# Performance work log

Measured on AMD Instinct MI355X. Metric: run time of the kernel, lower is better.

The kernel has to match this reference:

```python
import jax, jax.numpy as jnp
import numpy as np

EPS = 1e-5

def _ln(x, g, b):
    m = jnp.mean(x, axis=-1, keepdims=True)
    v = jnp.var(x, axis=-1, keepdims=True)
    return (x - m) / jnp.sqrt(v + EPS) * g + b

def setup_inputs() -> dict:
    key = jax.random.key(0)
    ks = jax.random.split(key, 16)
    B, N, CZ, C = 1, 512, 128, 16
    s_cz = 1.0 / np.sqrt(CZ)
    s_c = 1.0 / np.sqrt(C)
    def lin(k, fan_in, shape):
        return jax.random.uniform(k, shape, jnp.float32, -1.0, 1.0) / np.sqrt(fan_in)
    return {
        'x': jax.random.normal(ks[0], (B, N, N, CZ), jnp.float32),
        'Wa1': lin(ks[1], CZ, (CZ, C)), 'ba1': lin(ks[2], CZ, (C,)),
        'Wa2': lin(ks[3], CZ, (CZ, C)), 'ba2': lin(ks[4], CZ, (C,)),
        'Wb1': lin(ks[5], CZ, (CZ, C)), 'bb1': lin(ks[6], CZ, (C,)),
        'Wb2': lin(ks[7], CZ, (CZ, C)), 'bb2': lin(ks[8], CZ, (C,)),
        'ln2_g': jnp.ones((C,), jnp.float32), 'ln2_b': jnp.zeros((C,), jnp.float32),
        'Wg': lin(ks[9], CZ, (CZ, CZ)), 'bg': lin(ks[10], CZ, (CZ,)),
        'Wz': lin(ks[11], C, (C, CZ)), 'bz': lin(ks[12], C, (CZ,)),
    }

def reference(x, Wa1, ba1, Wa2, ba2, Wb1, bb1, Wb2, bb2, ln2_g, ln2_b, Wg, bg, Wz, bz):
    # NOTE: original code computes z=ln1(x) then overwrites z=x, so ln1 is a no-op.
    direction = 'outgoing'
    a = jax.nn.sigmoid((x @ Wa1 + ba1) * (x @ Wa2 + ba2))  # [B,N,N,c]
    b = jax.nn.sigmoid((x @ Wb1 + bb1) * (x @ Wb2 + bb2))  # [B,N,N,c]
    if direction == 'incoming':
        a = jnp.swapaxes(a, 1, 2)
        b = jnp.swapaxes(b, 1, 2)
    g = jax.nn.sigmoid(x @ Wg + bg)  # [B,N,N,c_z]
    # z[b,i,j,c] = sum_k a[b,i,k,c] * b[b,k,j,c]  (per-channel triangle matmul)
    z = jnp.einsum('bikc,bkjc->bijc', a, b)
    return g * (_ln(z, ln2_g, ln2_b) @ Wz + bz)
```

## Files before the change

### kernel.cpp

```cpp
#include <hip/hip_runtime.h>


#define NN 512
#define PP (NN*NN)
#define CZD 128
#define CD 16
#define LN_EPS 1e-5f

typedef unsigned short u16;
typedef __bf16 bf16x8 __attribute__((ext_vector_type(8)));
typedef float  f32x4  __attribute__((ext_vector_type(4)));

#define OFF_A  0u
#define OFF_B  8388608u
#define OFF_Z  16777216u
#define OFF_G  33554432u
#define OFF_WT 100663296u
#define OFF_BC 100712448u

__device__ __forceinline__ float bf2f(u16 u) {
    union { unsigned int i; float f; } v; v.i = ((unsigned int)u) << 16; return v.f;
}
__device__ __forceinline__ u16 f2bf(float f) {
    union { float f; unsigned int i; } v; v.f = f;
    unsigned int r = (v.i + 0x7FFFu + ((v.i >> 16) & 1u)) >> 16;
    return (u16)r;
}
__device__ __forceinline__ float sigmoidf(float x) { return 1.0f / (1.0f + __expf(-x)); }

__global__ void pack_w(const float* __restrict__ Wa1, const float* __restrict__ Wa2,
                       const float* __restrict__ Wb1, const float* __restrict__ Wb2,
                       const float* __restrict__ Wg,
                       const float* __restrict__ ba1, const float* __restrict__ ba2,
                       const float* __restrict__ bb1, const float* __restrict__ bb2,
                       const float* __restrict__ bg,
                       u16* __restrict__ wt, float* __restrict__ bc) {
    int idx = blockIdx.x * 256 + threadIdx.x;
    int n = idx >> 7, k = idx & 127;
    float v;
    if      (n < 16) v = Wa1[k * CD + n];
    else if (n < 32) v = Wa2[k * CD + (n - 16)];
    else if (n < 48) v = Wb1[k * CD + (n - 32)];
    else if (n < 64) v = Wb2[k * CD + (n - 48)];
    else             v = Wg [k * CZD + (n - 64)];
    wt[n * CZD + k] = f2bf(v);
    if (idx < 192) {
        float b;
        if      (idx < 16) b = ba1[idx];
        else if (idx < 32) b = ba2[idx - 16];
        else if (idx < 48) b = bb1[idx - 32];
        else if (idx < 64) b = bb2[idx - 48];
        else               b = bg [idx - 64];
        bc[idx] = b;
    }
}

__global__ __launch_bounds__(256) void proj_kernel(const float* __restrict__ x,
                                                   const u16* __restrict__ wt,
                                                   const float* __restrict__ bc,
                                                   u16* __restrict__ a_ws, u16* __restrict__ b_ws,
                                                   u16* __restrict__ g_ws) {
    __shared__ __align__(16) u16 Xlds[32][136];
    const int t = threadIdx.x;
    const int wave = t >> 6, lane = t & 63;
    const int l16 = lane & 15, quad = lane >> 4;
    const int rt = wave & 1, cg = wave >> 1;
    const long rowBase = (long)blockIdx.x * 32;

#pragma unroll
    for (int i = 0; i < 2; ++i) {
        int chunk = t + 256 * i;
        int r = chunk >> 4, ko = (chunk & 15) << 3;
        const float* xp = x + (rowBase + r) * CZD + ko;
        const float4 v0 = *reinterpret_cast<const float4*>(xp);
        const float4 v1 = *reinterpret_cast<const float4*>(xp + 4);
        u16 tmp[8] = { f2bf(v0.x), f2bf(v0.y), f2bf(v0.z), f2bf(v0.w),
                       f2bf(v1.x), f2bf(v1.y), f2bf(v1.z), f2bf(v1.w) };
        *reinterpret_cast<uint4*>(&Xlds[r][ko]) = *reinterpret_cast<const uint4*>(tmp);
    }
    bf16x8 wb[6][4];
#pragma unroll
    for (int ct = 0; ct < 6; ++ct) {
        int n = cg * 96 + ct * 16 + l16;
#pragma unroll
        for (int ks = 0; ks < 4; ++ks)
            wb[ct][ks] = *reinterpret_cast<const bf16x8*>(wt + n * CZD + ks * 32 + quad * 8);
    }
    __syncthreads();

    f32x4 acc[6];
#pragma unroll
    for (int ct = 0; ct < 6; ++ct) acc[ct] = (f32x4){0.f, 0.f, 0.f, 0.f};
#pragma unroll
    for (int ks = 0; ks < 4; ++ks) {
        bf16x8 af = *reinterpret_cast<const bf16x8*>(&Xlds[rt * 16 + l16][ks * 32 + quad * 8]);
#pragma unroll
        for (int ct = 0; ct < 6; ++ct)
            acc[ct] = __builtin_amdgcn_mfma_f32_16x16x32_bf16(af, wb[ct][ks], acc[ct], 0, 0, 0);
    }

    const int rl = rt * 16 + quad * 4;
    if (cg == 0) {
        const float b0 = bc[l16], b1 = bc[16 + l16], b2 = bc[32 + l16], b3 = bc[48 + l16];
        const float b4 = bc[64 + l16], b5 = bc[80 + l16];
#pragma unroll
        for (int r = 0; r < 4; ++r) {
            long pos = rowBase + rl + r;
            float av = sigmoidf((acc[0][r] + b0) * (acc[1][r] + b1));
            float bv = sigmoidf((acc[2][r] + b2) * (acc[3][r] + b3));
            a_ws[(long)l16 * PP + pos] = f2bf(av);
            b_ws[(long)l16 * PP + pos] = f2bf(bv);
            g_ws[pos * CZD + l16]      = f2bf(sigmoidf(acc[4][r] + b4));
            g_ws[pos * CZD + 16 + l16] = f2bf(sigmoidf(acc[5][r] + b5));
        }
    } else {
        float bb[6];
#pragma unroll
        for (int ct = 0; ct < 6; ++ct) bb[ct] = bc[96 + ct * 16 + l16];
#pragma unroll
        for (int r = 0; r < 4; ++r) {
            long pos = rowBase + rl + r;
#pragma unroll
            for (int ct = 0; ct < 6; ++ct)
                g_ws[pos * CZD + 32 + ct * 16 + l16] = f2bf(sigmoidf(acc[ct][r] + bb[ct]));
        }
    }
}

__global__ __launch_bounds__(256) void tri_kernel(const u16* __restrict__ a_ws,
                                                  const u16* __restrict__ b_ws,
                                                  float* __restrict__ z_ws) {
    __shared__ __align__(16) u16 Alds[64][72];
    __shared__ __align__(16) u16 Btl[64][72];
    const int t = threadIdx.x;
    const int wave = t >> 6, lane = t & 63, l16 = lane & 15, quad = lane >> 4;
    const int c = blockIdx.y;
    const int i0 = (blockIdx.x >> 3) * 64, j0 = (blockIdx.x & 7) * 64;
    const u16* Ap = a_ws + (long)c * PP;
    const u16* Bp = b_ws + (long)c * PP;

    f32x4 acc[4];
#pragma unroll
    for (int ct = 0; ct < 4; ++ct) acc[ct] = (f32x4){0.f, 0.f, 0.f, 0.f};

    for (int k0 = 0; k0 < NN; k0 += 64) {
#pragma unroll
        for (int i = 0; i < 2; ++i) {
            int chunk = t + 256 * i;
            int r = chunk >> 3, ko = (chunk & 7) << 3;
            uint4 v = *reinterpret_cast<const uint4*>(Ap + (long)(i0 + r) * NN + k0 + ko);
            *reinterpret_cast<uint4*>(&Alds[r][ko]) = v;
        }
#pragma unroll
        for (int i = 0; i < 2; ++i) {
            int chunk = t + 256 * i;
            int j = chunk & 63, kg = chunk >> 6;
            u16 tmp[8];
#pragma unroll
            for (int kk = 0; kk < 8; ++kk)
                tmp[kk] = Bp[(long)(k0 + kg * 8 + kk) * NN + j0 + j];
            *reinterpret_cast<uint4*>(&Btl[j][(kg ^ (j & 7)) << 3]) = *reinterpret_cast<uint4*>(tmp);
        }
        __syncthreads();
#pragma unroll
        for (int kk = 0; kk < 64; kk += 32) {
            bf16x8 af = *reinterpret_cast<const bf16x8*>(&Alds[wave * 16 + l16][kk + quad * 8]);
            int kc = (kk >> 3) + quad;
#pragma unroll
            for (int ct = 0; ct < 4; ++ct) {
                int n = ct * 16 + l16;
                bf16x8 bfv = *reinterpret_cast<const bf16x8*>(&Btl[n][(kc ^ (n & 7)) << 3]);
                acc[ct] = __builtin_amdgcn_mfma_f32_16x16x32_bf16(af, bfv, acc[ct], 0, 0, 0);
            }
        }
        __syncthreads();
    }
    float* Zp = z_ws + (long)c * PP;
#pragma unroll
    for (int ct = 0; ct < 4; ++ct)
#pragma unroll
        for (int r = 0; r < 4; ++r)
            Zp[(long)(i0 + wave * 16 + quad * 4 + r) * NN + j0 + ct * 16 + l16] = acc[ct][r];
}

__global__ __launch_bounds__(256) void out_kernel(const float* __restrict__ z_ws,
                                                  const u16* __restrict__ g_ws,
                                                  const float* __restrict__ Wz, const float* __restrict__ bz,
                                                  const float* __restrict__ lng, const float* __restrict__ lnb,
                                                  float* __restrict__ out) {
    __shared__ __align__(16) float zt[16][72];
    __shared__ __align__(16) float nl[64][20];
    __shared__ __align__(16) float wz[16][128];
    __shared__ float bzl[128];
    __shared__ float lg[16], lb[16];
    const int t = threadIdx.x;
    const long pos0 = (long)blockIdx.x * 64;

    {
        int cc = t >> 4, off = (t & 15) << 2;
        const float4 v = *reinterpret_cast<const float4*>(z_ws + (long)cc * PP + pos0 + off);
        *reinterpret_cast<float4*>(&zt[cc][off]) = v;
    }
#pragma unroll
    for (int i = 0; i < 8; ++i) {
        int idx = t + 256 * i;
        wz[idx >> 7][idx & 127] = Wz[idx];
    }
    if (t < 128)      bzl[t] = bz[t];
    else if (t < 144) lg[t - 128] = lng[t - 128];
    else if (t < 160) lb[t - 144] = lnb[t - 144];
    __syncthreads();

    {
        int p = t & 63, cgr = t >> 6;
        float m = 0.f;
#pragma unroll
        for (int c0 = 0; c0 < 16; ++c0) m += zt[c0][p];
        m *= (1.f / 16.f);
        float v = 0.f;
#pragma unroll
        for (int c0 = 0; c0 < 16; ++c0) { float d = zt[c0][p] - m; v += d * d; }
        v *= (1.f / 16.f);
        float s = rsqrtf(v + LN_EPS);
#pragma unroll
        for (int cc = 0; cc < 4; ++cc) {
            int c0 = cgr * 4 + cc;
            nl[p][c0] = (zt[c0][p] - m) * s * lg[c0] + lb[c0];
        }
    }
    __syncthreads();

    const int cz = t & 127, pg = t >> 7;
    float wzr[16];
#pragma unroll
    for (int c0 = 0; c0 < 16; ++c0) wzr[c0] = wz[c0][cz];
    const float bzv = bzl[cz];
#pragma unroll
    for (int pp2 = 0; pp2 < 32; ++pp2) {
        int p = pg * 32 + pp2;
        const float4* np = reinterpret_cast<const float4*>(&nl[p][0]);
        float y = bzv;
#pragma unroll
        for (int c4 = 0; c4 < 4; ++c4) {
            float4 nv = np[c4];
            y += nv.x * wzr[c4 * 4 + 0] + nv.y * wzr[c4 * 4 + 1] +
                 nv.z * wzr[c4 * 4 + 2] + nv.w * wzr[c4 * 4 + 3];
        }
        long o = (pos0 + p) * CZD + cz;
        float gv = bf2f(g_ws[o]);
        out[o] = gv * y;
    }
}

extern "C" void kernel_launch(void* const* d_in, const int* in_sizes, int n_in,
                              void* d_out, int out_size, void* d_ws, size_t ws_size,
                              hipStream_t stream) {
    const float* x   = (const float*)d_in[0];
    const float* Wa1 = (const float*)d_in[1];
    const float* ba1 = (const float*)d_in[2];
    const float* Wa2 = (const float*)d_in[3];
    const float* ba2 = (const float*)d_in[4];
    const float* Wb1 = (const float*)d_in[5];
    const float* bb1 = (const float*)d_in[6];
    const float* Wb2 = (const float*)d_in[7];
    const float* bb2 = (const float*)d_in[8];
    const float* lng = (const float*)d_in[9];
    const float* lnb = (const float*)d_in[10];
    const float* Wg  = (const float*)d_in[11];
    const float* bg  = (const float*)d_in[12];
    const float* Wz  = (const float*)d_in[13];
    const float* bz  = (const float*)d_in[14];
    float* out = (float*)d_out;
    char* ws = (char*)d_ws;
    u16*   a_ws = (u16*)(ws + OFF_A);
    u16*   b_ws = (u16*)(ws + OFF_B);
    float* z_ws = (float*)(ws + OFF_Z);
    u16*   g_ws = (u16*)(ws + OFF_G);
    u16*   wt   = (u16*)(ws + OFF_WT);
    float* bc   = (float*)(ws + OFF_BC);

    hipLaunchKernelGGL(pack_w, dim3(96), dim3(256), 0, stream,
                       Wa1, Wa2, Wb1, Wb2, Wg, ba1, ba2, bb1, bb2, bg, wt, bc);
    hipLaunchKernelGGL(proj_kernel, dim3(8192), dim3(256), 0, stream, x, wt, bc, a_ws, b_ws, g_ws);
    hipLaunchKernelGGL(tri_kernel, dim3(64, 16), dim3(256), 0, stream, a_ws, b_ws, z_ws);
    hipLaunchKernelGGL(out_kernel, dim3(4096), dim3(256), 0, stream, z_ws, g_ws, Wz, bz, lng, lnb, out);
}
```

Baseline: 377.8 us.

## Restructure projection kernel with LDS-staged weights and coalesced transposed output stores

The projection kernel now processes 128 positions per 512-thread block. It stages the packed weights and the bf16-converted x tile in XOR-swizzled shared memory, and each wave computes all 192 output columns for its 16 rows. Results for a, b and g are written to shared memory first and then stored to global memory as 16-byte coalesced writes. Previously a and b were written as scattered 2-byte stores into channel-major layout. The change adds 80KB of dynamic LDS per block, which limits occupancy, and adds extra barriers.

Measured after the change: 321.9 us. -14.8%, faster.

```diff
diff --git a/kernel.cpp b/kernel.cpp
--- a/kernel.cpp
+++ b/kernel.cpp
@@ -27,6 +27,10 @@
     return (u16)r;
 }
 __device__ __forceinline__ float sigmoidf(float x) { return 1.0f / (1.0f + __expf(-x)); }
+
+__device__ __forceinline__ int swz(int row, int bytecol) {
+    return row * 256 + (bytecol ^ ((row & 7) << 4));
+}
 
 __global__ void pack_w(const float* __restrict__ Wa1, const float* __restrict__ Wa2,
                        const float* __restrict__ Wb1, const float* __restrict__ Wb2,
@@ -55,75 +59,93 @@
     }
 }
 
-__global__ __launch_bounds__(256) void proj_kernel(const float* __restrict__ x,
-                                                   const u16* __restrict__ wt,
-                                                   const float* __restrict__ bc,
-                                                   u16* __restrict__ a_ws, u16* __restrict__ b_ws,
-                                                   u16* __restrict__ g_ws) {
-    __shared__ __align__(16) u16 Xlds[32][136];
+__global__ __launch_bounds__(512, 4) void proj_kernel(const float* __restrict__ x,
+                                                      const u16* __restrict__ wt,
+                                                      const float* __restrict__ bc,
+                                                      u16* __restrict__ a_ws, u16* __restrict__ b_ws,
+                                                      u16* __restrict__ g_ws) {
+    extern __shared__ __align__(16) char lds[];
+    char* Wl = lds;
+    char* Xl = lds + 49152;
+    char* aT = lds;
+    char* bT = lds + 4096;
+    char* gT = lds + 49152;
     const int t = threadIdx.x;
-    const int wave = t >> 6, lane = t & 63;
-    const int l16 = lane & 15, quad = lane >> 4;
-    const int rt = wave & 1, cg = wave >> 1;
-    const long rowBase = (long)blockIdx.x * 32;
-
-#pragma unroll
-    for (int i = 0; i < 2; ++i) {
-        int chunk = t + 256 * i;
-        int r = chunk >> 4, ko = (chunk & 15) << 3;
-        const float* xp = x + (rowBase + r) * CZD + ko;
-        const float4 v0 = *reinterpret_cast<const float4*>(xp);
-        const float4 v1 = *reinterpret_cast<const float4*>(xp + 4);
-        u16 tmp[8] = { f2bf(v0.x), f2bf(v0.y), f2bf(v0.z), f2bf(v0.w),
-                       f2bf(v1.x), f2bf(v1.y), f2bf(v1.z), f2bf(v1.w) };
-        *reinterpret_cast<uint4*>(&Xlds[r][ko]) = *reinterpret_cast<const uint4*>(tmp);
-    }
-    bf16x8 wb[6][4];
-#pragma unroll
-    for (int ct = 0; ct < 6; ++ct) {
-        int n = cg * 96 + ct * 16 + l16;
-#pragma unroll
-        for (int ks = 0; ks < 4; ++ks)
-            wb[ct][ks] = *reinterpret_cast<const bf16x8*>(wt + n * CZD + ks * 32 + quad * 8);
-    }
-    __syncthreads();
-
-    f32x4 acc[6];
-#pragma unroll
-    for (int ct = 0; ct < 6; ++ct) acc[ct] = (f32x4){0.f, 0.f, 0.f, 0.f};
-#pragma unroll
-    for (int ks = 0; ks < 4; ++ks) {
-        bf16x8 af = *reinterpret_cast<const bf16x8*>(&Xlds[rt * 16 + l16][ks * 32 + quad * 8]);
-#pragma unroll
-        for (int ct = 0; ct < 6; ++ct)
-            acc[ct] = __builtin_amdgcn_mfma_f32_16x16x32_bf16(af, wb[ct][ks], acc[ct], 0, 0, 0);
-    }
-
-    const int rl = rt * 16 + quad * 4;
-    if (cg == 0) {
-        const float b0 = bc[l16], b1 = bc[16 + l16], b2 = bc[32 + l16], b3 = bc[48 + l16];
-        const float b4 = bc[64 + l16], b5 = bc[80 + l16];
+    const int wv = t >> 6, lane = t & 63, l16 = lane & 15, quad = lane >> 4;
+    const long pos0 = (long)blockIdx.x * 128;
+
+#pragma unroll
+    for (int i = 0; i < 6; ++i) {
+        int c = t + 512 * i;
+        int n = c >> 4, g = c & 15;
+        uint4 v = *reinterpret_cast<const uint4*>(wt + n * CZD + g * 8);
+        *reinterpret_cast<uint4*>(Wl + swz(n, g * 16)) = v;
+    }
+#pragma unroll
+    for (int i = 0; i < 8; ++i) {
+        int c = t + 512 * i;
+        int r = c >> 5, c4 = c & 31;
+        const float4 v = *reinterpret_cast<const float4*>(x + (pos0 + r) * CZD + c4 * 4);
+        u16 tmp[4] = { f2bf(v.x), f2bf(v.y), f2bf(v.z), f2bf(v.w) };
+        *reinterpret_cast<uint2*>(Xl + swz(r, c4 * 8)) = *reinterpret_cast<const uint2*>(tmp);
+    }
+    __syncthreads();
+
+    f32x4 acc[12];
+#pragma unroll
+    for (int ct = 0; ct < 12; ++ct) acc[ct] = (f32x4){0.f, 0.f, 0.f, 0.f};
+    bf16x8 af[4];
+#pragma unroll
+    for (int ks = 0; ks < 4; ++ks)
+        af[ks] = *reinterpret_cast<const bf16x8*>(Xl + swz(wv * 16 + l16, ks * 64 + quad * 16));
+#pragma unroll
+    for (int ks = 0; ks < 4; ++ks)
+#pragma unroll
+        for (int ct = 0; ct < 12; ++ct) {
+            bf16x8 wb = *reinterpret_cast<const bf16x8*>(Wl + swz(ct * 16 + l16, ks * 64 + quad * 16));
+            acc[ct] = __builtin_amdgcn_mfma_f32_16x16x32_bf16(af[ks], wb, acc[ct], 0, 0, 0);
+        }
+    __syncthreads();
+
+    {
+        const float ba1 = bc[l16], ba2 = bc[16 + l16], bb1 = bc[32 + l16], bb2 = bc[48 + l16];
+        u16 av[4], bv[4];
 #pragma unroll
         for (int r = 0; r < 4; ++r) {
-            long pos = rowBase + rl + r;
-            float av = sigmoidf((acc[0][r] + b0) * (acc[1][r] + b1));
-            float bv = sigmoidf((acc[2][r] + b2) * (acc[3][r] + b3));
-            a_ws[(long)l16 * PP + pos] = f2bf(av);
-            b_ws[(long)l16 * PP + pos] = f2bf(bv);
-            g_ws[pos * CZD + l16]      = f2bf(sigmoidf(acc[4][r] + b4));
-            g_ws[pos * CZD + 16 + l16] = f2bf(sigmoidf(acc[5][r] + b5));
-        }
+            av[r] = f2bf(sigmoidf((acc[0][r] + ba1) * (acc[1][r] + ba2)));
+            bv[r] = f2bf(sigmoidf((acc[2][r] + bb1) * (acc[3][r] + bb2)));
+        }
+        *reinterpret_cast<uint2*>(aT + swz(l16, wv * 32 + quad * 8)) = *reinterpret_cast<const uint2*>(av);
+        *reinterpret_cast<uint2*>(bT + swz(l16, wv * 32 + quad * 8)) = *reinterpret_cast<const uint2*>(bv);
+#pragma unroll
+        for (int ct = 0; ct < 8; ++ct) {
+            const float bgv = bc[64 + ct * 16 + l16];
+#pragma unroll
+            for (int r = 0; r < 4; ++r) {
+                int pos = wv * 16 + quad * 4 + r;
+                *reinterpret_cast<u16*>(gT + swz(pos, ct * 32 + l16 * 2)) =
+                    f2bf(sigmoidf(acc[4 + ct][r] + bgv));
+            }
+        }
+    }
+    __syncthreads();
+
+    if (t < 256) {
+        int ch = t >> 4, i = t & 15;
+        uint4 v = *reinterpret_cast<const uint4*>(aT + swz(ch, i * 16));
+        *reinterpret_cast<uint4*>(a_ws + (long)ch * PP + pos0 + i * 8) = v;
     } else {
-        float bb[6];
-#pragma unroll
-        for (int ct = 0; ct < 6; ++ct) bb[ct] = bc[96 + ct * 16 + l16];
-#pragma unroll
-        for (int r = 0; r < 4; ++r) {
-            long pos = rowBase + rl + r;
-#pragma unroll
-            for (int ct = 0; ct < 6; ++ct)
-                g_ws[pos * CZD + 32 + ct * 16 + l16] = f2bf(sigmoidf(acc[ct][r] + bb[ct]));
-        }
+        int u = t - 256;
+        int ch = u >> 4, i = u & 15;
+        uint4 v = *reinterpret_cast<const uint4*>(bT + swz(ch, i * 16));
+        *reinterpret_cast<uint4*>(b_ws + (long)ch * PP + pos0 + i * 8) = v;
+    }
+#pragma unroll
+    for (int i = 0; i < 4; ++i) {
+        int c = t + 512 * i;
+        int pos = c >> 4, g = c & 15;
+        uint4 v = *reinterpret_cast<const uint4*>(gT + swz(pos, g * 16));
+        *reinterpret_cast<uint4*>(g_ws + (pos0 + pos) * CZD + g * 8) = v;
     }
 }
 
@@ -281,7 +303,7 @@
 
     hipLaunchKernelGGL(pack_w, dim3(96), dim3(256), 0, stream,
                        Wa1, Wa2, Wb1, Wb2, Wg, ba1, ba2, bb1, bb2, bg, wt, bc);
-    hipLaunchKernelGGL(proj_kernel, dim3(8192), dim3(256), 0, stream, x, wt, bc, a_ws, b_ws, g_ws);
+    hipLaunchKernelGGL(proj_kernel, dim3(2048), dim3(512), 81920, stream, x, wt, bc, a_ws, b_ws, g_ws);
     hipLaunchKernelGGL(tri_kernel, dim3(64, 16), dim3(256), 0, stream, a_ws, b_ws, z_ws);
     hipLaunchKernelGGL(out_kernel, dim3(4096), dim3(256), 0, stream, z_ws, g_ws, Wz, bz, lng, lnb, out);
 }
```
